# Kernel tuning notes

Hardware: AMD Instinct MI355X
Metric: run time of the kernel (lower is better)

The kernel has to match this reference:

```python
import jax, jax.numpy as jnp
import numpy as np

N_NODES = 100000
N_EDGES = 3200000
D_IN = 128


def setup_inputs() -> dict:
    key = jax.random.key(0)
    k1, k2, k3, k4 = jax.random.split(key, 4)
    x = jax.random.normal(k1, (N_NODES, D_IN), dtype=jnp.float32)
    edge_index = jax.random.randint(k2, (2, N_EDGES), 0, N_NODES, dtype=jnp.int64)
    W1 = jax.random.normal(k3, (D_IN, 16), dtype=jnp.float32) * (1.0 / np.sqrt(D_IN))
    b1 = jnp.zeros((16,), dtype=jnp.float32)
    W2 = jax.random.normal(k4, (16, 2), dtype=jnp.float32) * (1.0 / np.sqrt(16))
    b2 = jnp.zeros((2,), dtype=jnp.float32)
    return {"x": x, "edge_index": edge_index, "W1": W1, "b1": b1, "W2": W2, "b2": b2}


def _gcn_norm(edge_index, n_nodes):
    # Add self-loops, then symmetric degree normalization (PyG gcn_norm).
    loops = jnp.arange(n_nodes, dtype=edge_index.dtype)
    row = jnp.concatenate([edge_index[0], loops])  # source
    col = jnp.concatenate([edge_index[1], loops])  # target
    ones = jnp.ones(row.shape[0], dtype=jnp.float32)
    deg = jax.ops.segment_sum(ones, col, num_segments=n_nodes)
    dis = jnp.where(deg > 0, jax.lax.rsqrt(deg), 0.0)  # deg^{-1/2}
    norm = dis[row] * dis[col]  # [E+N]
    return row, col, norm


def _gcn_conv(x, row, col, norm, W, b, n_nodes):
    h = x @ W  # transform first (PyG order): [N, out]
    msgs = h[row] * norm[:, None]  # gather from source, scale
    agg = jax.ops.segment_sum(msgs, col, num_segments=n_nodes)  # scatter-add to target
    return agg + b


def reference(x, edge_index, W1, b1, W2, b2):
    n = x.shape[0]
    row, col, norm = _gcn_norm(edge_index, n)
    h = _gcn_conv(x, row, col, norm, W1, b1, n)
    h = jax.nn.relu(h)
    h = _gcn_conv(h, row, col, norm, W2, b2, n)
    return jax.nn.log_softmax(h, axis=1)
```

## Files before the change

### kernel.cpp

```cpp
#include <hip/hip_runtime.h>
#include <hip/hip_fp16.h>

#define DIN 128
#define BSH 7
#define BSIZE 128
#define NBMAX 800
#define CAP 4480
#define CHUNK 8192

__global__ __launch_bounds__(256) void init_kernel(int* __restrict__ cur, int NB) {
    int i = blockIdx.x * 256 + threadIdx.x;
    if (i < NB) cur[i] = i * CAP;
}

__global__ __launch_bounds__(256) void place_kernel(const int* __restrict__ row,
                                                    const int* __restrict__ col,
                                                    int* __restrict__ cur,
                                                    int* __restrict__ sp, int E, int NB) {
    __shared__ int pk[CHUNK];
    __shared__ unsigned short bkid[CHUNK];
    __shared__ int lcnt[NBMAX], lstart[NBMAX], gofs[NBMAX], lcur[NBMAX];
    __shared__ int sst[256];
    int t = threadIdx.x;
    int e0 = blockIdx.x * CHUNK;
    int cnt = min(CHUNK, E - e0);

    for (int i = t; i < NBMAX; i += 256) { lcnt[i] = 0; lcur[i] = 0; }
    __syncthreads();
    for (int i = t; i < cnt; i += 256)
        atomicAdd(&lcnt[col[e0 + i] >> BSH], 1);
    __syncthreads();
    int b4 = t * 4;
    int v0 = (b4 + 0 < NBMAX) ? lcnt[b4 + 0] : 0;
    int v1 = (b4 + 1 < NBMAX) ? lcnt[b4 + 1] : 0;
    int v2 = (b4 + 2 < NBMAX) ? lcnt[b4 + 2] : 0;
    int v3 = (b4 + 3 < NBMAX) ? lcnt[b4 + 3] : 0;
    int tot = v0 + v1 + v2 + v3;
    sst[t] = tot;
    __syncthreads();
    for (int d = 1; d < 256; d <<= 1) {
        int tmp = (t >= d) ? sst[t - d] : 0;
        __syncthreads();
        sst[t] += tmp;
        __syncthreads();
    }
    int ex = sst[t] - tot;
    if (b4 + 0 < NBMAX) lstart[b4 + 0] = ex;
    if (b4 + 1 < NBMAX) lstart[b4 + 1] = ex + v0;
    if (b4 + 2 < NBMAX) lstart[b4 + 2] = ex + v0 + v1;
    if (b4 + 3 < NBMAX) lstart[b4 + 3] = ex + v0 + v1 + v2;
    __syncthreads();
    for (int b = t; b < NB; b += 256) {
        int c = lcnt[b];
        int gb = c ? atomicAdd(&cur[b], c) : 0;
        gofs[b] = gb - lstart[b];
    }
    __syncthreads();
    for (int i = t; i < cnt; i += 256) {
        int r  = row[e0 + i];
        int cc = col[e0 + i];
        int b  = cc >> BSH;
        int rk = atomicAdd(&lcur[b], 1);
        int pos = lstart[b] + rk;
        pk[pos]   = ((cc & (BSIZE - 1)) << 17) | r;
        bkid[pos] = (unsigned short)b;
    }
    __syncthreads();
    for (int i = t; i < cnt; i += 256)
        sp[gofs[bkid[i]] + i] = pk[i];
}

__global__ __launch_bounds__(256) void bdeg_kernel(const int* __restrict__ sp,
                                                   const int* __restrict__ cur,
                                                   float* __restrict__ dis, int N) {
    __shared__ int lcnt[BSIZE];
    int b = blockIdx.x;
    int t = threadIdx.x;
    int cntb = cur[b] - b * CAP;
    const int* src = sp + (size_t)b * CAP;
    if (t < BSIZE) lcnt[t] = 0;
    __syncthreads();
    int n4 = cntb >> 2;
    const int4* src4 = (const int4*)src;
    for (int i = t; i < n4; i += 256) {
        int4 v = src4[i];
        atomicAdd(&lcnt[v.x >> 17], 1);
        atomicAdd(&lcnt[v.y >> 17], 1);
        atomicAdd(&lcnt[v.z >> 17], 1);
        atomicAdd(&lcnt[v.w >> 17], 1);
    }
    for (int i = (n4 << 2) + t; i < cntb; i += 256)
        atomicAdd(&lcnt[src[i] >> 17], 1);
    __syncthreads();
    if (t < BSIZE) {
        int gt = b * BSIZE + t;
        if (gt < N) dis[gt] = rsqrtf((float)lcnt[t] + 1.0f);
    }
}

__global__ __launch_bounds__(1024) void bscan_kernel(const int* __restrict__ cur,
                                                     int* __restrict__ bbase, int NB) {
    __shared__ int s[1024];
    int t = threadIdx.x;
    int v = (t < NB) ? (cur[t] - t * CAP) : 0;
    s[t] = v;
    __syncthreads();
    for (int d = 1; d < 1024; d <<= 1) {
        int tmp = (t >= d) ? s[t - d] : 0;
        __syncthreads();
        s[t] += tmp;
        __syncthreads();
    }
    if (t < NB) bbase[t] = s[t] - v;
    if (t == NB - 1) bbase[NB] = s[t];
}

__global__ __launch_bounds__(256) void xw1_kernel(const float* __restrict__ x,
                                                  const float* __restrict__ W1,
                                                  const float* __restrict__ dis,
                                                  __half* __restrict__ hp, int N) {
    __shared__ float xs[64 * 132];
    __shared__ float wt[16 * 132];
    int t = threadIdx.x;
    int base = blockIdx.x * 64;
    for (int i = t; i < DIN * 16; i += 256) {
        int d = i >> 4, k = i & 15;
        wt[k * 132 + d] = W1[i];
    }
    int nrow = min(64, N - base);
    for (int i = t; i < 64 * 32; i += 256) {
        int r = i >> 5, c4 = i & 31;
        float4 v = make_float4(0.f, 0.f, 0.f, 0.f);
        if (r < nrow) v = *(const float4*)(x + (size_t)(base + r) * DIN + c4 * 4);
        *(float4*)(xs + r * 132 + c4 * 4) = v;
    }
    __syncthreads();
    int np = t >> 3;
    int kp = t & 7;
    int n0 = np * 2, k0 = kp * 2;
    const float4* xa = (const float4*)(xs + n0 * 132);
    const float4* xb = (const float4*)(xs + (n0 + 1) * 132);
    const float4* wa = (const float4*)(wt + k0 * 132);
    const float4* wb = (const float4*)(wt + (k0 + 1) * 132);
    float a00 = 0.f, a01 = 0.f, a10 = 0.f, a11 = 0.f;
    #pragma unroll 8
    for (int d4 = 0; d4 < 32; d4++) {
        float4 va = xa[d4], vb = xb[d4], u0 = wa[d4], u1 = wb[d4];
        a00 += va.x*u0.x + va.y*u0.y + va.z*u0.z + va.w*u0.w;
        a01 += va.x*u1.x + va.y*u1.y + va.z*u1.z + va.w*u1.w;
        a10 += vb.x*u0.x + vb.y*u0.y + vb.z*u0.z + vb.w*u0.w;
        a11 += vb.x*u1.x + vb.y*u1.y + vb.z*u1.z + vb.w*u1.w;
    }
    int n = base + n0;
    if (n < N) {
        float d = dis[n];
        hp[(size_t)n * 16 + k0 + 0] = __float2half(a00 * d);
        hp[(size_t)n * 16 + k0 + 1] = __float2half(a01 * d);
    }
    n++;
    if (n < N) {
        float d = dis[n];
        hp[(size_t)n * 16 + k0 + 0] = __float2half(a10 * d);
        hp[(size_t)n * 16 + k0 + 1] = __float2half(a11 * d);
    }
}

__global__ __launch_bounds__(256) void bsg1_kernel(const int* __restrict__ sp,
                                                   const int* __restrict__ bbase,
                                                   const float* __restrict__ dis,
                                                   const __half2* __restrict__ hp2,
                                                   const float* __restrict__ b1,
                                                   const float* __restrict__ W2,
                                                   int* __restrict__ srt,
                                                   int* __restrict__ off,
                                                   float* __restrict__ gp, int N) {
    __shared__ int spk[CAP];
    __shared__ int ss[CAP];
    __shared__ int lcnt[BSIZE], lstart[BSIZE], lcur[BSIZE], sc[BSIZE];
    int b = blockIdx.x;
    int t = threadIdx.x;
    int base = bbase[b];
    int cntb = bbase[b + 1] - base;
    const int* src = sp + (size_t)b * CAP;
    if (t < BSIZE) { lcnt[t] = 0; lcur[t] = 0; }
    __syncthreads();
    for (int i = t; i < cntb; i += 256) {
        int v = src[i];
        spk[i] = v;
        atomicAdd(&lcnt[v >> 17], 1);
    }
    __syncthreads();
    int v = (t < BSIZE) ? lcnt[t] : 0;
    if (t < BSIZE) sc[t] = v;
    __syncthreads();
    for (int d = 1; d < BSIZE; d <<= 1) {
        int tmp = (t < BSIZE && t >= d) ? sc[t - d] : 0;
        __syncthreads();
        if (t < BSIZE) sc[t] += tmp;
        __syncthreads();
    }
    if (t < BSIZE) lstart[t] = sc[t] - v;
    __syncthreads();
    for (int i = t; i < cntb; i += 256) {
        int vv = spk[i];
        int lt = vv >> 17;
        int rk = atomicAdd(&lcur[lt], 1);
        ss[lstart[lt] + rk] = vv & 0x1FFFF;
    }
    __syncthreads();
    for (int i = t; i < cntb; i += 256) srt[base + i] = ss[i];
    if (t < BSIZE) {
        int gt = b * BSIZE + t;
        if (gt < N) off[gt] = base + lstart[t];
    }
    int k2  = t & 7;
    int ltg = t >> 3;
    #pragma unroll
    for (int r4 = 0; r4 < 4; r4++) {
        int lt = r4 * 32 + ltg;
        int gt = b * BSIZE + lt;
        if (gt < N) {
            int j0 = lstart[lt];
            int j1 = j0 + lcnt[lt];
            float2 acc0 = __half22float2(hp2[(size_t)gt * 8 + k2]);
            float2 acc1 = make_float2(0.f, 0.f);
            float2 acc2 = make_float2(0.f, 0.f);
            float2 acc3 = make_float2(0.f, 0.f);
            int j = j0;
            for (; j + 3 < j1; j += 4) {
                int r0 = ss[j + 0], r1 = ss[j + 1], r2 = ss[j + 2], r3 = ss[j + 3];
                float2 h0 = __half22float2(hp2[(size_t)r0 * 8 + k2]);
                float2 h1 = __half22float2(hp2[(size_t)r1 * 8 + k2]);
                float2 h2 = __half22float2(hp2[(size_t)r2 * 8 + k2]);
                float2 h3 = __half22float2(hp2[(size_t)r3 * 8 + k2]);
                acc0.x += h0.x; acc0.y += h0.y;
                acc1.x += h1.x; acc1.y += h1.y;
                acc2.x += h2.x; acc2.y += h2.y;
                acc3.x += h3.x; acc3.y += h3.y;
            }
            for (; j < j1; j++) {
                int r = ss[j];
                float2 hv = __half22float2(hp2[(size_t)r * 8 + k2]);
                acc0.x += hv.x; acc0.y += hv.y;
            }
            float2 acc = make_float2(acc0.x + acc1.x + acc2.x + acc3.x,
                                     acc0.y + acc1.y + acc2.y + acc3.y);
            float d = dis[gt];
            int k0 = k2 * 2;
            float v0 = fmaxf(fmaf(acc.x, d, b1[k0 + 0]), 0.0f);
            float v1 = fmaxf(fmaf(acc.y, d, b1[k0 + 1]), 0.0f);
            float p0 = v0 * W2[k0 * 2 + 0] + v1 * W2[k0 * 2 + 2];
            float p1 = v0 * W2[k0 * 2 + 1] + v1 * W2[k0 * 2 + 3];
            p0 += __shfl_xor(p0, 1); p1 += __shfl_xor(p1, 1);
            p0 += __shfl_xor(p0, 2); p1 += __shfl_xor(p1, 2);
            p0 += __shfl_xor(p0, 4); p1 += __shfl_xor(p1, 4);
            if (k2 == 0) *(float2*)(gp + (size_t)gt * 2) = make_float2(p0 * d, p1 * d);
        }
    }
}

__global__ __launch_bounds__(256) void g2_kernel(const int* __restrict__ srt,
                                                 const int* __restrict__ off,
                                                 const float* __restrict__ dis,
                                                 const float* __restrict__ gp,
                                                 const float* __restrict__ b2,
                                                 float* __restrict__ out, int N, int E) {
    int t = blockIdx.x * 256 + threadIdx.x;
    int c    = t >> 2;
    int slot = t & 3;
    if (c >= N) return;
    int j0 = off[c];
    int j1 = (c == N - 1) ? E : off[c + 1];
    float a0 = 0.0f, a1v = 0.0f;
    for (int j = j0 + slot; j < j1; j += 4) {
        int r = srt[j];
        float2 gv = *(const float2*)(gp + (size_t)r * 2);
        a0  += gv.x;
        a1v += gv.y;
    }
    a0 += __shfl_xor(a0, 1); a1v += __shfl_xor(a1v, 1);
    a0 += __shfl_xor(a0, 2); a1v += __shfl_xor(a1v, 2);
    if (slot == 0) {
        float2 self = *(const float2*)(gp + (size_t)c * 2);
        float d = dis[c];
        float o0 = (a0  + self.x) * d + b2[0];
        float o1 = (a1v + self.y) * d + b2[1];
        float m = fmaxf(o0, o1);
        float lse = m + logf(expf(o0 - m) + expf(o1 - m));
        *(float2*)(out + (size_t)c * 2) = make_float2(o0 - lse, o1 - lse);
    }
}

extern "C" void kernel_launch(void* const* d_in, const int* in_sizes, int n_in,
                              void* d_out, int out_size, void* d_ws, size_t ws_size,
                              hipStream_t stream) {
    const float* x  = (const float*)d_in[0];
    const int*   ei = (const int*)d_in[1];
    const float* W1 = (const float*)d_in[2];
    const float* b1 = (const float*)d_in[3];
    const float* W2 = (const float*)d_in[4];
    const float* b2 = (const float*)d_in[5];
    float* out = (float*)d_out;

    const int N = in_sizes[0] / DIN;
    const int E = in_sizes[1] / 2;
    const int* row = ei;
    const int* col = ei + E;
    const int NB = (N + BSIZE - 1) / BSIZE;

    int*    cur   = (int*)d_ws;
    int*    bbase = cur + NBMAX;
    float*  dis   = (float*)(bbase + NBMAX + 1);
    int*    off   = (int*)(dis + N);
    int*    srt   = off + N;
    int*    sp    = srt + E;
    __half* hp    = (__half*)(sp + (size_t)NB * CAP);
    float*  gp    = (float*)(hp + (size_t)N * 16);

    init_kernel <<<(NB + 255) / 256, 256, 0, stream>>>(cur, NB);
    place_kernel<<<(E + CHUNK - 1) / CHUNK, 256, 0, stream>>>(row, col, cur, sp, E, NB);
    bdeg_kernel <<<NB, 256, 0, stream>>>(sp, cur, dis, N);
    bscan_kernel<<<1, 1024, 0, stream>>>(cur, bbase, NB);
    xw1_kernel  <<<(N + 63) / 64, 256, 0, stream>>>(x, W1, dis, hp, N);
    bsg1_kernel <<<NB, 256, 0, stream>>>(sp, bbase, dis, (const __half2*)hp, b1, W2, srt, off, gp, N);
    g2_kernel   <<<(int)(((size_t)N * 4 + 255) / 256), 256, 0, stream>>>(srt, off, dis, gp, b2, out, N, E);
}
```

Baseline: 215.2 us.

## Fuse layer-1 aggregation and layer-2 gather into one cooperative kernel with grid sync

Merges the bucket-sort/layer-1 kernel and the layer-2 gather kernel into a single cooperative launch. The sorted per-bucket source lists stay in shared memory across a grid.sync instead of being written to and reread from global srt/off arrays, which removes the separate scan kernel and that global round-trip. The place kernel also moves to 512 threads per block. In exchange, all 782 blocks must be co-resident for the cooperative launch, the grid barrier adds cost, and large shared-memory use per block caps occupancy.

Result: slower. 312.3 us (+45.1%).

```diff
diff --git a/kernel.cpp b/kernel.cpp
--- a/kernel.cpp
+++ b/kernel.cpp
@@ -1,5 +1,8 @@
 #include <hip/hip_runtime.h>
 #include <hip/hip_fp16.h>
+#include <hip/hip_cooperative_groups.h>
+
+namespace cg = cooperative_groups;
 
 #define DIN 128
 #define BSH 7
@@ -7,56 +10,53 @@
 #define NBMAX 800
 #define CAP 4480
 #define CHUNK 8192
+#define PB 512
 
 __global__ __launch_bounds__(256) void init_kernel(int* __restrict__ cur, int NB) {
     int i = blockIdx.x * 256 + threadIdx.x;
     if (i < NB) cur[i] = i * CAP;
 }
 
-__global__ __launch_bounds__(256) void place_kernel(const int* __restrict__ row,
-                                                    const int* __restrict__ col,
-                                                    int* __restrict__ cur,
-                                                    int* __restrict__ sp, int E, int NB) {
+__global__ __launch_bounds__(PB) void place_kernel(const int* __restrict__ row,
+                                                   const int* __restrict__ col,
+                                                   int* __restrict__ cur,
+                                                   int* __restrict__ sp, int E, int NB) {
     __shared__ int pk[CHUNK];
     __shared__ unsigned short bkid[CHUNK];
     __shared__ int lcnt[NBMAX], lstart[NBMAX], gofs[NBMAX], lcur[NBMAX];
-    __shared__ int sst[256];
+    __shared__ int sst[PB];
     int t = threadIdx.x;
     int e0 = blockIdx.x * CHUNK;
     int cnt = min(CHUNK, E - e0);
 
-    for (int i = t; i < NBMAX; i += 256) { lcnt[i] = 0; lcur[i] = 0; }
-    __syncthreads();
-    for (int i = t; i < cnt; i += 256)
+    for (int i = t; i < NBMAX; i += PB) { lcnt[i] = 0; lcur[i] = 0; }
+    __syncthreads();
+    for (int i = t; i < cnt; i += PB)
         atomicAdd(&lcnt[col[e0 + i] >> BSH], 1);
     __syncthreads();
-    int b4 = t * 4;
-    int v0 = (b4 + 0 < NBMAX) ? lcnt[b4 + 0] : 0;
-    int v1 = (b4 + 1 < NBMAX) ? lcnt[b4 + 1] : 0;
-    int v2 = (b4 + 2 < NBMAX) ? lcnt[b4 + 2] : 0;
-    int v3 = (b4 + 3 < NBMAX) ? lcnt[b4 + 3] : 0;
-    int tot = v0 + v1 + v2 + v3;
+    int b2i = t * 2;
+    int v0 = (b2i + 0 < NBMAX) ? lcnt[b2i + 0] : 0;
+    int v1 = (b2i + 1 < NBMAX) ? lcnt[b2i + 1] : 0;
+    int tot = v0 + v1;
     sst[t] = tot;
     __syncthreads();
-    for (int d = 1; d < 256; d <<= 1) {
+    for (int d = 1; d < PB; d <<= 1) {
         int tmp = (t >= d) ? sst[t - d] : 0;
         __syncthreads();
         sst[t] += tmp;
         __syncthreads();
     }
     int ex = sst[t] - tot;
-    if (b4 + 0 < NBMAX) lstart[b4 + 0] = ex;
-    if (b4 + 1 < NBMAX) lstart[b4 + 1] = ex + v0;
-    if (b4 + 2 < NBMAX) lstart[b4 + 2] = ex + v0 + v1;
-    if (b4 + 3 < NBMAX) lstart[b4 + 3] = ex + v0 + v1 + v2;
-    __syncthreads();
-    for (int b = t; b < NB; b += 256) {
+    if (b2i + 0 < NBMAX) lstart[b2i + 0] = ex;
+    if (b2i + 1 < NBMAX) lstart[b2i + 1] = ex + v0;
+    __syncthreads();
+    for (int b = t; b < NB; b += PB) {
         int c = lcnt[b];
         int gb = c ? atomicAdd(&cur[b], c) : 0;
         gofs[b] = gb - lstart[b];
     }
     __syncthreads();
-    for (int i = t; i < cnt; i += 256) {
+    for (int i = t; i < cnt; i += PB) {
         int r  = row[e0 + i];
         int cc = col[e0 + i];
         int b  = cc >> BSH;
@@ -66,7 +66,7 @@
         bkid[pos] = (unsigned short)b;
     }
     __syncthreads();
-    for (int i = t; i < cnt; i += 256)
+    for (int i = t; i < cnt; i += PB)
         sp[gofs[bkid[i]] + i] = pk[i];
 }
 
@@ -96,23 +96,6 @@
         int gt = b * BSIZE + t;
         if (gt < N) dis[gt] = rsqrtf((float)lcnt[t] + 1.0f);
     }
-}
-
-__global__ __launch_bounds__(1024) void bscan_kernel(const int* __restrict__ cur,
-                                                     int* __restrict__ bbase, int NB) {
-    __shared__ int s[1024];
-    int t = threadIdx.x;
-    int v = (t < NB) ? (cur[t] - t * CAP) : 0;
-    s[t] = v;
-    __syncthreads();
-    for (int d = 1; d < 1024; d <<= 1) {
-        int tmp = (t >= d) ? s[t - d] : 0;
-        __syncthreads();
-        s[t] += tmp;
-        __syncthreads();
-    }
-    if (t < NB) bbase[t] = s[t] - v;
-    if (t == NB - 1) bbase[NB] = s[t];
 }
 
 __global__ __launch_bounds__(256) void xw1_kernel(const float* __restrict__ x,
@@ -165,22 +148,22 @@
     }
 }
 
-__global__ __launch_bounds__(256) void bsg1_kernel(const int* __restrict__ sp,
-                                                   const int* __restrict__ bbase,
-                                                   const float* __restrict__ dis,
-                                                   const __half2* __restrict__ hp2,
-                                                   const float* __restrict__ b1,
-                                                   const float* __restrict__ W2,
-                                                   int* __restrict__ srt,
-                                                   int* __restrict__ off,
-                                                   float* __restrict__ gp, int N) {
+__global__ __launch_bounds__(256, 4) void fuse_kernel(const int* __restrict__ sp,
+                                                      const int* __restrict__ cur,
+                                                      const float* __restrict__ dis,
+                                                      const __half2* __restrict__ hp2,
+                                                      const float* __restrict__ b1,
+                                                      const float* __restrict__ W2,
+                                                      const float* __restrict__ b2,
+                                                      float* __restrict__ gp,
+                                                      float* __restrict__ out, int N) {
     __shared__ int spk[CAP];
     __shared__ int ss[CAP];
     __shared__ int lcnt[BSIZE], lstart[BSIZE], lcur[BSIZE], sc[BSIZE];
+    cg::grid_group grid = cg::this_grid();
     int b = blockIdx.x;
     int t = threadIdx.x;
-    int base = bbase[b];
-    int cntb = bbase[b + 1] - base;
+    int cntb = cur[b] - b * CAP;
     const int* src = sp + (size_t)b * CAP;
     if (t < BSIZE) { lcnt[t] = 0; lcur[t] = 0; }
     __syncthreads();
@@ -208,11 +191,6 @@
         ss[lstart[lt] + rk] = vv & 0x1FFFF;
     }
     __syncthreads();
-    for (int i = t; i < cntb; i += 256) srt[base + i] = ss[i];
-    if (t < BSIZE) {
-        int gt = b * BSIZE + t;
-        if (gt < N) off[gt] = base + lstart[t];
-    }
     int k2  = t & 7;
     int ltg = t >> 3;
     #pragma unroll
@@ -257,37 +235,38 @@
             if (k2 == 0) *(float2*)(gp + (size_t)gt * 2) = make_float2(p0 * d, p1 * d);
         }
     }
-}
-
-__global__ __launch_bounds__(256) void g2_kernel(const int* __restrict__ srt,
-                                                 const int* __restrict__ off,
-                                                 const float* __restrict__ dis,
-                                                 const float* __restrict__ gp,
-                                                 const float* __restrict__ b2,
-                                                 float* __restrict__ out, int N, int E) {
-    int t = blockIdx.x * 256 + threadIdx.x;
-    int c    = t >> 2;
-    int slot = t & 3;
-    if (c >= N) return;
-    int j0 = off[c];
-    int j1 = (c == N - 1) ? E : off[c + 1];
-    float a0 = 0.0f, a1v = 0.0f;
-    for (int j = j0 + slot; j < j1; j += 4) {
-        int r = srt[j];
-        float2 gv = *(const float2*)(gp + (size_t)r * 2);
-        a0  += gv.x;
-        a1v += gv.y;
-    }
-    a0 += __shfl_xor(a0, 1); a1v += __shfl_xor(a1v, 1);
-    a0 += __shfl_xor(a0, 2); a1v += __shfl_xor(a1v, 2);
-    if (slot == 0) {
-        float2 self = *(const float2*)(gp + (size_t)c * 2);
-        float d = dis[c];
-        float o0 = (a0  + self.x) * d + b2[0];
-        float o1 = (a1v + self.y) * d + b2[1];
-        float m = fmaxf(o0, o1);
-        float lse = m + logf(expf(o0 - m) + expf(o1 - m));
-        *(float2*)(out + (size_t)c * 2) = make_float2(o0 - lse, o1 - lse);
+    grid.sync();
+    int lt2 = t >> 1;
+    int sl  = t & 1;
+    int gt2 = b * BSIZE + lt2;
+    if (gt2 < N) {
+        int j0 = lstart[lt2];
+        int j1 = j0 + lcnt[lt2];
+        float a0 = 0.f, a1v = 0.f, c0 = 0.f, c1v = 0.f;
+        int j = j0 + sl;
+        for (; j + 2 < j1; j += 4) {
+            int ra = ss[j], rb = ss[j + 2];
+            float2 ga = *(const float2*)(gp + (size_t)ra * 2);
+            float2 gb = *(const float2*)(gp + (size_t)rb * 2);
+            a0 += ga.x; a1v += ga.y;
+            c0 += gb.x; c1v += gb.y;
+        }
+        for (; j < j1; j += 2) {
+            int r = ss[j];
+            float2 gv = *(const float2*)(gp + (size_t)r * 2);
+            a0 += gv.x; a1v += gv.y;
+        }
+        a0 += c0; a1v += c1v;
+        a0 += __shfl_xor(a0, 1); a1v += __shfl_xor(a1v, 1);
+        if (sl == 0) {
+            float2 self = *(const float2*)(gp + (size_t)gt2 * 2);
+            float d = dis[gt2];
+            float o0 = (a0  + self.x) * d + b2[0];
+            float o1 = (a1v + self.y) * d + b2[1];
+            float m = fmaxf(o0, o1);
+            float lse = m + logf(expf(o0 - m) + expf(o1 - m));
+            *(float2*)(out + (size_t)gt2 * 2) = make_float2(o0 - lse, o1 - lse);
+        }
     }
 }
 
@@ -308,20 +287,22 @@
     const int* col = ei + E;
     const int NB = (N + BSIZE - 1) / BSIZE;
 
-    int*    cur   = (int*)d_ws;
-    int*    bbase = cur + NBMAX;
-    float*  dis   = (float*)(bbase + NBMAX + 1);
-    int*    off   = (int*)(dis + N);
-    int*    srt   = off + N;
-    int*    sp    = srt + E;
-    __half* hp    = (__half*)(sp + (size_t)NB * CAP);
-    float*  gp    = (float*)(hp + (size_t)N * 16);
+    int*    cur = (int*)d_ws;
+    float*  dis = (float*)(cur + NBMAX);
+    int*    sp  = (int*)(dis + N);
+    __half* hp  = (__half*)(sp + (size_t)NB * CAP);
+    float*  gp  = (float*)(hp + (size_t)N * 16);
 
     init_kernel <<<(NB + 255) / 256, 256, 0, stream>>>(cur, NB);
-    place_kernel<<<(E + CHUNK - 1) / CHUNK, 256, 0, stream>>>(row, col, cur, sp, E, NB);
+    place_kernel<<<(E + CHUNK - 1) / CHUNK, PB, 0, stream>>>(row, col, cur, sp, E, NB);
     bdeg_kernel <<<NB, 256, 0, stream>>>(sp, cur, dis, N);
-    bscan_kernel<<<1, 1024, 0, stream>>>(cur, bbase, NB);
     xw1_kernel  <<<(N + 63) / 64, 256, 0, stream>>>(x, W1, dis, hp, N);
-    bsg1_kernel <<<NB, 256, 0, stream>>>(sp, bbase, dis, (const __half2*)hp, b1, W2, srt, off, gp, N);
-    g2_kernel   <<<(int)(((size_t)N * 4 + 255) / 256), 256, 0, stream>>>(srt, off, dis, gp, b2, out, N, E);
-}
+
+    const __half2* hp2 = (const __half2*)hp;
+    int Nv = N;
+    void* args[] = { (void*)&sp, (void*)&cur, (void*)&dis, (void*)&hp2,
+                     (void*)&b1, (void*)&W2, (void*)&b2, (void*)&gp,
+                     (void*)&out, (void*)&Nv };
+    hipLaunchCooperativeKernel((const void*)fuse_kernel, dim3(NB), dim3(256),
+                               args, 0, stream);
+}
```
